# Performance work log

Hardware: AMD Instinct MI355X
Metric: run time of the kernel (lower is better)

The kernel has to match this reference:

```python
import jax, jax.numpy as jnp
import numpy as np
import math

L = 6      # num transformer layers
D = 128    # hidden_dim
H = 8      # heads
C = D // H # per-head dim (concat -> H*C == hidden_dim so residual add works)
F = 9      # node_features
OUT = 3    # output_dim
B, S, NN = 2, 128, 64
N = B * S * NN
E = 262144


def setup_inputs() -> dict:
    key = jax.random.key(0)
    ks = jax.random.split(key, 16)
    sc = 0.02
    g = lambda k, shp: jax.random.normal(k, shp, jnp.float32) * sc

    x = jax.random.normal(ks[0], (N, F), jnp.float32)
    edge_index = jax.random.randint(ks[1], (2, E), 0, N, dtype=jnp.int32)

    # sinusoidal positional encoding buffer [S, D]
    pos = np.arange(S, dtype=np.float32)[:, None]
    div = np.exp(np.arange(0, D, 2, dtype=np.float32) * (-math.log(10000.0) / D))
    pe = np.zeros((S, D), np.float32)
    pe[:, 0::2] = np.sin(pos * div)
    pe[:, 1::2] = np.cos(pos * div)

    return dict(
        x=x, edge_index=edge_index, pe=jnp.asarray(pe),
        Win=g(ks[2], (F, D)), bin_=jnp.zeros((D,), jnp.float32),
        Wq=g(ks[3], (L, D, D)), bq=jnp.zeros((L, D), jnp.float32),
        Wk=g(ks[4], (L, D, D)), bk=jnp.zeros((L, D), jnp.float32),
        Wv=g(ks[5], (L, D, D)), bv=jnp.zeros((L, D), jnp.float32),
        Ws=g(ks[6], (L, D, D)), bs=jnp.zeros((L, D), jnp.float32),
        Wb=g(ks[7], (L, 3 * D, 1)), bb=jnp.zeros((L, 1), jnp.float32),
        ln_g=jnp.ones((L, D), jnp.float32), ln_b=jnp.zeros((L, D), jnp.float32),
        Wo1=g(ks[8], (D, D // 2)), bo1=jnp.zeros((D // 2,), jnp.float32),
        Wo2=g(ks[9], (D // 2, OUT)), bo2=jnp.zeros((OUT,), jnp.float32),
        batch_size=B, seq_len=S, num_nodes=NN,
    )


def _layer_norm(x, g, b, eps=1e-5):
    mu = x.mean(-1, keepdims=True)
    var = ((x - mu) ** 2).mean(-1, keepdims=True)
    return (x - mu) / jnp.sqrt(var + eps) * g + b


def _transformer_conv(h, src, dst, Wq, bq, Wk, bk, Wv, bv, Ws, bs, Wb, bb):
    # PyG TransformerConv (beta=True, concat): edge gather -> per-head dot scores
    # -> scatter-softmax over incoming edges per dst node -> scatter-add aggregate.
    n = h.shape[0]
    q = (h @ Wq + bq).reshape(n, H, C)
    k = (h @ Wk + bk).reshape(n, H, C)
    v = (h @ Wv + bv).reshape(n, H, C)
    scores = jnp.einsum('ehc,ehc->eh', q[dst], k[src]) / math.sqrt(C)  # [E,H]
    m = jax.ops.segment_max(scores, dst, num_segments=n)               # [N,H]
    ex = jnp.exp(scores - jax.lax.stop_gradient(m)[dst])
    denom = jax.ops.segment_sum(ex, dst, num_segments=n)
    alpha = ex / (denom[dst] + 1e-16)                                  # [E,H]
    msg = (v[src] * alpha[:, :, None]).reshape(-1, H * C)              # [E,D]
    agg = jax.ops.segment_sum(msg, dst, num_segments=n)                # [N,D]
    xr = h @ Ws + bs                                                   # skip branch
    beta = jax.nn.sigmoid(jnp.concatenate([agg, xr, agg - xr], -1) @ Wb + bb)
    return beta * xr + (1.0 - beta) * agg


def reference(x, edge_index, pe, Win, bin_, Wq, bq, Wk, bk, Wv, bv, Ws, bs,
              Wb, bb, ln_g, ln_b, Wo1, bo1, Wo2, bo2,
              batch_size, seq_len, num_nodes):
    src, dst = edge_index[0], edge_index[1]
    d = Win.shape[1]
    h = x @ Win + bin_
    # add temporal positional encoding per timestep
    h = (h.reshape(batch_size, seq_len, num_nodes, d)
         + pe[:seq_len][None, :, None, :]).reshape(-1, d)
    for i in range(Wq.shape[0]):
        hn = _transformer_conv(h, src, dst, Wq[i], bq[i], Wk[i], bk[i],
                               Wv[i], bv[i], Ws[i], bs[i], Wb[i], bb[i])
        h = _layer_norm(h + hn, ln_g[i], ln_b[i])
    return jax.nn.relu(h @ Wo1 + bo1) @ Wo2 + bo2
```

## Files before the change

kernel.cpp:

```cpp
#include <hip/hip_runtime.h>

#define NNODES 16384
#define EDGES  262144
#define DH     128
#define NH     8
#define CH     16
#define NL     6
#define SEQ    128
#define NNPG   64

typedef short bf16x8 __attribute__((ext_vector_type(8)));
typedef float f32x4 __attribute__((ext_vector_type(4)));
typedef float f32x2 __attribute__((ext_vector_type(2)));

static __device__ __forceinline__ unsigned short f2bf(float f) {
  unsigned u = __float_as_uint(f);
  u += 0x7FFFu + ((u >> 16) & 1u);
  return (unsigned short)(u >> 16);
}
static __device__ __forceinline__ float bfl(unsigned u) { return __uint_as_float(u << 16); }
static __device__ __forceinline__ float bfh(unsigned u) { return __uint_as_float(u & 0xffff0000u); }

__global__ __launch_bounds__(128) void k_input(const float* __restrict__ x,
    const float* __restrict__ Win, const float* __restrict__ bin,
    const float* __restrict__ pe, float* __restrict__ h,
    unsigned short* __restrict__ hb) {
  const int n = blockIdx.x, d = threadIdx.x;
  __shared__ float xs[9];
  if (d < 9) xs[d] = x[n * 9 + d];
  __syncthreads();
  float acc = bin[d];
#pragma unroll
  for (int f = 0; f < 9; ++f) acc = fmaf(xs[f], Win[f * DH + d], acc);
  const float val = acc + pe[((n / NNPG) % SEQ) * DH + d];
  h[n * DH + d] = val;
  hb[n * DH + d] = f2bf(val);
}

__global__ __launch_bounds__(256) void k_count(const int* __restrict__ ei,
                                               int* __restrict__ cnt) {
  const int e = blockIdx.x * 256 + threadIdx.x;
  atomicAdd(&cnt[ei[EDGES + e]], 1);
}

__global__ __launch_bounds__(1024) void k_scan(int* __restrict__ cnt,
                                               int* __restrict__ row_start) {
  __shared__ int part[1024];
  const int t = threadIdx.x;
  int loc[16];
  int s = 0;
  const int base = t * 16;
#pragma unroll
  for (int i = 0; i < 16; ++i) { loc[i] = cnt[base + i]; s += loc[i]; }
  part[t] = s;
  __syncthreads();
  for (int off = 1; off < 1024; off <<= 1) {
    int add = (t >= off) ? part[t - off] : 0;
    __syncthreads();
    part[t] += add;
    __syncthreads();
  }
  int run = (t == 0) ? 0 : part[t - 1];
#pragma unroll
  for (int i = 0; i < 16; ++i) {
    row_start[base + i] = run;
    run += loc[i];
    cnt[base + i] = 0;
  }
  if (t == 0) row_start[NNODES] = EDGES;
}

__global__ __launch_bounds__(256) void k_fill(const int* __restrict__ ei,
    const int* __restrict__ row_start, int* __restrict__ cursor,
    int* __restrict__ csr_src) {
  const int e = blockIdx.x * 256 + threadIdx.x;
  const int d = ei[EDGES + e];
  csr_src[row_start[d] + atomicAdd(&cursor[d], 1)] = ei[e];
}

__global__ __launch_bounds__(64) void k_wconv(const float* __restrict__ Wq,
    const float* __restrict__ Wk, const float* __restrict__ Wv,
    const float* __restrict__ Ws, unsigned short* __restrict__ Wf) {
  const int bid = blockIdx.x;
  const int layer = bid >> 7, rem = bid & 127;
  const int mat = rem >> 5, tile = rem & 31;
  const int nt = tile >> 2, kt = tile & 3;
  const int lane = threadIdx.x;
  const float* W = ((mat == 0) ? Wq : (mat == 1) ? Wk : (mat == 2) ? Wv : Ws)
                   + layer * DH * DH;
  const int n = nt * 16 + (lane & 15);
  const int k0 = kt * 32 + (lane >> 4) * 8;
  unsigned pk[4];
#pragma unroll
  for (int jj = 0; jj < 4; ++jj) {
    const unsigned lo = f2bf(W[(k0 + 2 * jj) * DH + n]);
    const unsigned hi = f2bf(W[(k0 + 2 * jj + 1) * DH + n]);
    pk[jj] = lo | (hi << 16);
  }
  uint4 o = {pk[0], pk[1], pk[2], pk[3]};
  *(uint4*)&Wf[(((layer * 4 + mat) * 32 + tile) * 64 + lane) * 8] = o;
}

__global__ __launch_bounds__(256) void k_gemm(const unsigned short* __restrict__ hb,
    const unsigned short* __restrict__ Wf,
    const float* __restrict__ bq, const float* __restrict__ bk,
    const float* __restrict__ bv, const float* __restrict__ bs,
    unsigned short* __restrict__ qb, unsigned char* __restrict__ kb8,
    unsigned char* __restrict__ vb8, float* __restrict__ xr) {
  const int mt = blockIdx.x;
  const int wv = threadIdx.x >> 6, lane = threadIdx.x & 63;
  const int g = blockIdx.y * 4 + wv;
  const int mat = g >> 1, nbase = (g & 1) * 64;
  const unsigned short* Wm = Wf + mat * 16384;
  const float* bias = (mat == 0) ? bq : (mat == 1) ? bk : (mat == 2) ? bv : bs;
  const int m0 = lane & 15, quad = lane >> 4;
  const int nt0 = (g & 1) * 4;

  const f32x4 z = {0.f, 0.f, 0.f, 0.f};
  f32x4 acc[2][4] = {{z, z, z, z}, {z, z, z, z}};
#pragma unroll
  for (int kt = 0; kt < 4; ++kt) {
    const bf16x8 a0 = *(const bf16x8*)&hb[(mt * 32 + m0) * DH + kt * 32 + quad * 8];
    const bf16x8 a1 = *(const bf16x8*)&hb[(mt * 32 + 16 + m0) * DH + kt * 32 + quad * 8];
#pragma unroll
    for (int j = 0; j < 4; ++j) {
      const bf16x8 b = *(const bf16x8*)&Wm[(((nt0 + j) * 4 + kt) * 64 + lane) * 8];
      acc[0][j] = __builtin_amdgcn_mfma_f32_16x16x32_bf16(a0, b, acc[0][j], 0, 0, 0);
      acc[1][j] = __builtin_amdgcn_mfma_f32_16x16x32_bf16(a1, b, acc[1][j], 0, 0, 0);
    }
  }
  unsigned char* __restrict__ f8dst = (mat == 1) ? kb8 : vb8;
#pragma unroll
  for (int half = 0; half < 2; ++half) {
#pragma unroll
    for (int j = 0; j < 4; ++j) {
      const int col = nbase + j * 16 + m0;
      const float bvv = bias[col];
#pragma unroll
      for (int r = 0; r < 4; ++r) {
        const float val = acc[half][j][r] + bvv;
        const int row = mt * 32 + half * 16 + quad * 4 + r;
        if (mat == 0) {
          qb[row * DH + col] = f2bf(val);
        } else if (mat == 3) {
          xr[row * DH + col] = val;
        } else {
          const float nbv = __shfl_xor(val, 1);
          if ((lane & 1) == 0) {
            const int pk = __builtin_amdgcn_cvt_pk_fp8_f32(val, nbv, 0, false);
            *(unsigned short*)&f8dst[row * DH + col] = (unsigned short)pk;
          }
        }
      }
    }
  }
}

__device__ __forceinline__ void load16bf(const unsigned short* __restrict__ p, float* r) {
  const uint4 a = *(const uint4*)p;
  const uint4 b = *(const uint4*)(p + 8);
  r[0] = bfl(a.x); r[1] = bfh(a.x); r[2] = bfl(a.y); r[3] = bfh(a.y);
  r[4] = bfl(a.z); r[5] = bfh(a.z); r[6] = bfl(a.w); r[7] = bfh(a.w);
  r[8] = bfl(b.x); r[9] = bfh(b.x); r[10] = bfl(b.y); r[11] = bfh(b.y);
  r[12] = bfl(b.z); r[13] = bfh(b.z); r[14] = bfl(b.w); r[15] = bfh(b.w);
}

__device__ __forceinline__ void decode16f8(const uint4 u, float* r) {
  f32x2 t;
  t = __builtin_amdgcn_cvt_pk_f32_fp8(u.x, false); r[0] = t[0]; r[1] = t[1];
  t = __builtin_amdgcn_cvt_pk_f32_fp8(u.x, true);  r[2] = t[0]; r[3] = t[1];
  t = __builtin_amdgcn_cvt_pk_f32_fp8(u.y, false); r[4] = t[0]; r[5] = t[1];
  t = __builtin_amdgcn_cvt_pk_f32_fp8(u.y, true);  r[6] = t[0]; r[7] = t[1];
  t = __builtin_amdgcn_cvt_pk_f32_fp8(u.z, false); r[8] = t[0]; r[9] = t[1];
  t = __builtin_amdgcn_cvt_pk_f32_fp8(u.z, true);  r[10] = t[0]; r[11] = t[1];
  t = __builtin_amdgcn_cvt_pk_f32_fp8(u.w, false); r[12] = t[0]; r[13] = t[1];
  t = __builtin_amdgcn_cvt_pk_f32_fp8(u.w, true);  r[14] = t[0]; r[15] = t[1];
}

__device__ __forceinline__ void edge_acc_m(const uint4 ku, const uint4 vu, bool valid,
    const float* __restrict__ qr, float* __restrict__ acc, float& denom) {
  float kr[16], vr[16];
  decode16f8(ku, kr);
  float dot = 0.f;
#pragma unroll
  for (int c = 0; c < 16; ++c) dot = fmaf(qr[c], kr[c], dot);
  const float ex = valid ? __expf(dot * 0.25f) : 0.f;
  denom += ex;
  decode16f8(vu, vr);
#pragma unroll
  for (int c = 0; c < 16; ++c) acc[c] = fmaf(ex, vr[c], acc[c]);
}

__global__ __launch_bounds__(256) void k_attn_epi(const unsigned short* __restrict__ qb,
    const unsigned char* __restrict__ kb8, const unsigned char* __restrict__ vb8,
    const int* __restrict__ row_start, const int* __restrict__ csr_src,
    float* __restrict__ h, unsigned short* __restrict__ hb,
    const float* __restrict__ xr,
    const float* __restrict__ Wb, const float* __restrict__ bb,
    const float* __restrict__ ln_g, const float* __restrict__ ln_b) {
  const int wv = threadIdx.x >> 6, lane = threadIdx.x & 63;
  const int n = blockIdx.x * 4 + wv;
  const int es = lane >> 3, hd = lane & 7;
  const int beg = row_start[n], end = row_start[n + 1];
  int j = beg + es;
  int idx[4];
#pragma unroll
  for (int t = 0; t < 4; ++t) {
    const int jt = j + 8 * t;
    idx[t] = (jt < end) ? csr_src[jt] : -1;
  }
  float qr[16];
  load16bf(&qb[n * DH + hd * CH], qr);
  uint4 kf[4], vf[4];
#pragma unroll
  for (int t = 0; t < 4; ++t) {
    const int s = (idx[t] >= 0) ? idx[t] : 0;
    kf[t] = *(const uint4*)&kb8[s * DH + hd * CH];
    vf[t] = *(const uint4*)&vb8[s * DH + hd * CH];
  }
  float acc[16] = {};
  float denom = 0.f;
#pragma unroll
  for (int t = 0; t < 4; ++t)
    edge_acc_m(kf[t], vf[t], idx[t] >= 0, qr, acc, denom);
  for (j = beg + es + 32; j < end; j += 8) {
    const int s = csr_src[j];
    const uint4 ku = *(const uint4*)&kb8[s * DH + hd * CH];
    const uint4 vu = *(const uint4*)&vb8[s * DH + hd * CH];
    edge_acc_m(ku, vu, true, qr, acc, denom);
  }
#pragma unroll
  for (int off = 8; off <= 32; off <<= 1) {
    denom += __shfl_xor(denom, off);
#pragma unroll
    for (int c = 0; c < 16; ++c) acc[c] += __shfl_xor(acc[c], off);
  }
  const float inv = 1.f / (denom + 1e-16f);
  float o0 = 0.f, o1 = 0.f;
#pragma unroll
  for (int c = 0; c < 8; ++c) {
    if (es == c) { o0 = acc[2 * c]; o1 = acc[2 * c + 1]; }
  }
  const int d0 = hd * CH + es * 2;
  const float ax = o0 * inv, ay = o1 * inv;
  const float2 r = *(const float2*)&xr[n * DH + d0];
  const float2 w0 = *(const float2*)&Wb[d0];
  const float2 w1 = *(const float2*)&Wb[DH + d0];
  const float2 w2 = *(const float2*)&Wb[2 * DH + d0];
  float p = ax * w0.x + ay * w0.y + r.x * w1.x + r.y * w1.y
          + (ax - r.x) * w2.x + (ay - r.y) * w2.y;
#pragma unroll
  for (int off = 1; off <= 32; off <<= 1) p += __shfl_xor(p, off);
  const float beta = 1.f / (1.f + __expf(-(p + bb[0])));
  const float2 hv = *(const float2*)&h[n * DH + d0];
  const float t0 = hv.x + beta * r.x + (1.f - beta) * ax;
  const float t1 = hv.y + beta * r.y + (1.f - beta) * ay;
  float sum = t0 + t1, sq = t0 * t0 + t1 * t1;
#pragma unroll
  for (int off = 1; off <= 32; off <<= 1) {
    sum += __shfl_xor(sum, off);
    sq  += __shfl_xor(sq, off);
  }
  const float mu = sum * (1.f / DH);
  const float rinv = rsqrtf(sq * (1.f / DH) - mu * mu + 1e-5f);
  const float2 g = *(const float2*)&ln_g[d0];
  const float2 b = *(const float2*)&ln_b[d0];
  float2 o = {(t0 - mu) * rinv * g.x + b.x, (t1 - mu) * rinv * g.y + b.y};
  *(float2*)&h[n * DH + d0] = o;
  const unsigned lo = f2bf(o.x), hi = f2bf(o.y);
  *(unsigned*)&hb[n * DH + d0] = lo | (hi << 16);
}

__global__ __launch_bounds__(256) void k_final(const float* __restrict__ h,
    const float* __restrict__ Wo1, const float* __restrict__ bo1,
    const float* __restrict__ Wo2, const float* __restrict__ bo2,
    float* __restrict__ out) {
  __shared__ float hs[4][DH];
  const int lane = threadIdx.x & 63, wid = threadIdx.x >> 6;
  const int n = blockIdx.x * 4 + wid;
  const float2 hv = *(const float2*)&h[n * DH + lane * 2];
  hs[wid][lane * 2] = hv.x;
  hs[wid][lane * 2 + 1] = hv.y;
  __syncthreads();
  float m = bo1[lane];
#pragma unroll 16
  for (int d = 0; d < DH; ++d) m = fmaf(hs[wid][d], Wo1[d * 64 + lane], m);
  m = fmaxf(m, 0.f);
  float o0 = m * Wo2[lane * 3 + 0];
  float o1 = m * Wo2[lane * 3 + 1];
  float o2 = m * Wo2[lane * 3 + 2];
#pragma unroll
  for (int off = 32; off; off >>= 1) {
    o0 += __shfl_xor(o0, off);
    o1 += __shfl_xor(o1, off);
    o2 += __shfl_xor(o2, off);
  }
  if (lane == 0) {
    out[n * 3 + 0] = o0 + bo2[0];
    out[n * 3 + 1] = o1 + bo2[1];
    out[n * 3 + 2] = o2 + bo2[2];
  }
}

extern "C" void kernel_launch(void* const* d_in, const int* in_sizes, int n_in,
                              void* d_out, int out_size, void* d_ws, size_t ws_size,
                              hipStream_t stream) {
  const float* x   = (const float*)d_in[0];
  const int*   ei  = (const int*)d_in[1];
  const float* pe  = (const float*)d_in[2];
  const float* Win = (const float*)d_in[3];
  const float* bin = (const float*)d_in[4];
  const float* Wq  = (const float*)d_in[5];
  const float* bq  = (const float*)d_in[6];
  const float* Wk  = (const float*)d_in[7];
  const float* bk  = (const float*)d_in[8];
  const float* Wv  = (const float*)d_in[9];
  const float* bv  = (const float*)d_in[10];
  const float* Wsk = (const float*)d_in[11];
  const float* bs  = (const float*)d_in[12];
  const float* Wb  = (const float*)d_in[13];
  const float* bb  = (const float*)d_in[14];
  const float* lng = (const float*)d_in[15];
  const float* lnb = (const float*)d_in[16];
  const float* Wo1 = (const float*)d_in[17];
  const float* bo1 = (const float*)d_in[18];
  const float* Wo2 = (const float*)d_in[19];
  const float* bo2 = (const float*)d_in[20];

  const size_t NU = (size_t)NNODES * DH;
  char* base = (char*)d_ws;
  float* h   = (float*)base;                  base += NU * 4;
  float* xr  = (float*)base;                  base += NU * 4;
  unsigned short* hb = (unsigned short*)base; base += NU * 2;
  unsigned short* qb = (unsigned short*)base; base += NU * 2;
  unsigned char* kb8 = (unsigned char*)base;  base += NU;
  unsigned char* vb8 = (unsigned char*)base;  base += NU;
  unsigned short* Wf = (unsigned short*)base; base += (size_t)NL * 4 * 16384 * 2;
  int* row_start = (int*)base;                base += (NNODES + 1) * 4;
  int* cnt       = (int*)base;                base += NNODES * 4;
  int* csr_src   = (int*)base;

  (void)hipMemsetAsync(cnt, 0, NNODES * sizeof(int), stream);
  k_count<<<EDGES / 256, 256, 0, stream>>>(ei, cnt);
  k_scan<<<1, 1024, 0, stream>>>(cnt, row_start);
  k_fill<<<EDGES / 256, 256, 0, stream>>>(ei, row_start, cnt, csr_src);
  k_wconv<<<NL * 128, 64, 0, stream>>>(Wq, Wk, Wv, Wsk, Wf);
  k_input<<<NNODES, 128, 0, stream>>>(x, Win, bin, pe, h, hb);
  for (int l = 0; l < NL; ++l) {
    k_gemm<<<dim3(NNODES / 32, 2), 256, 0, stream>>>(
        hb, Wf + (size_t)l * 4 * 16384,
        bq + l * DH, bk + l * DH, bv + l * DH, bs + l * DH, qb, kb8, vb8, xr);
    k_attn_epi<<<NNODES / 4, 256, 0, stream>>>(qb, kb8, vb8, row_start, csr_src,
                                               h, hb, xr, Wb + l * 3 * DH, bb + l,
                                               lng + l * DH, lnb + l * DH);
  }
  k_final<<<NNODES / 4, 256, 0, stream>>>(h, Wo1, bo1, Wo2, bo2, (float*)d_out);
}
```

Measured before the change: 390.5 us.

## Split edge score computation into a separate edge-parallel kernel

Edge attention scores (q·k and exp) move out of the per-destination-node attention kernel into a new k_score kernel that runs in parallel over CSR edges, using a new csr_dst array built in k_fill. Scores go to a global buffer of E×H floats, which the aggregation kernel reads back while gathering V. The aim is to balance load across edges rather than nodes with uneven degree. The cost is an extra launch per layer and an 8 MB round-trip of scores through memory.

```diff
diff --git a/kernel.cpp b/kernel.cpp
--- a/kernel.cpp
+++ b/kernel.cpp
@@ -72,10 +72,12 @@
 
 __global__ __launch_bounds__(256) void k_fill(const int* __restrict__ ei,
     const int* __restrict__ row_start, int* __restrict__ cursor,
-    int* __restrict__ csr_src) {
+    int* __restrict__ csr_src, int* __restrict__ csr_dst) {
   const int e = blockIdx.x * 256 + threadIdx.x;
   const int d = ei[EDGES + e];
-  csr_src[row_start[d] + atomicAdd(&cursor[d], 1)] = ei[e];
+  const int pos = row_start[d] + atomicAdd(&cursor[d], 1);
+  csr_src[pos] = ei[e];
+  csr_dst[pos] = d;
 }
 
 __global__ __launch_bounds__(64) void k_wconv(const float* __restrict__ Wq,
@@ -177,22 +179,35 @@
   t = __builtin_amdgcn_cvt_pk_f32_fp8(u.w, true);  r[14] = t[0]; r[15] = t[1];
 }
 
-__device__ __forceinline__ void edge_acc_m(const uint4 ku, const uint4 vu, bool valid,
-    const float* __restrict__ qr, float* __restrict__ acc, float& denom) {
-  float kr[16], vr[16];
+__global__ __launch_bounds__(256) void k_score(const unsigned short* __restrict__ qb,
+    const unsigned char* __restrict__ kb8, const int* __restrict__ csr_src,
+    const int* __restrict__ csr_dst, float* __restrict__ ex) {
+  const int wv = threadIdx.x >> 6, lane = threadIdx.x & 63;
+  const int el = lane >> 3, hd = lane & 7;
+  const int j = blockIdx.x * 32 + wv * 8 + el;
+  const int s = csr_src[j];
+  const int d = csr_dst[j];
+  float qr[16], kr[16];
+  load16bf(&qb[d * DH + hd * CH], qr);
+  const uint4 ku = *(const uint4*)&kb8[s * DH + hd * CH];
   decode16f8(ku, kr);
   float dot = 0.f;
 #pragma unroll
   for (int c = 0; c < 16; ++c) dot = fmaf(qr[c], kr[c], dot);
-  const float ex = valid ? __expf(dot * 0.25f) : 0.f;
-  denom += ex;
+  ex[j * 8 + hd] = __expf(dot * 0.25f);
+}
+
+__device__ __forceinline__ void v_acc(const uint4 vu, float w,
+    float* __restrict__ acc, float& denom) {
+  float vr[16];
   decode16f8(vu, vr);
-#pragma unroll
-  for (int c = 0; c < 16; ++c) acc[c] = fmaf(ex, vr[c], acc[c]);
-}
-
-__global__ __launch_bounds__(256) void k_attn_epi(const unsigned short* __restrict__ qb,
-    const unsigned char* __restrict__ kb8, const unsigned char* __restrict__ vb8,
+  denom += w;
+#pragma unroll
+  for (int c = 0; c < 16; ++c) acc[c] = fmaf(w, vr[c], acc[c]);
+}
+
+__global__ __launch_bounds__(256) void k_attn_epi(
+    const unsigned char* __restrict__ vb8, const float* __restrict__ ex,
     const int* __restrict__ row_start, const int* __restrict__ csr_src,
     float* __restrict__ h, unsigned short* __restrict__ hb,
     const float* __restrict__ xr,
@@ -202,32 +217,30 @@
   const int n = blockIdx.x * 4 + wv;
   const int es = lane >> 3, hd = lane & 7;
   const int beg = row_start[n], end = row_start[n + 1];
-  int j = beg + es;
+  const int j0 = beg + es;
   int idx[4];
 #pragma unroll
   for (int t = 0; t < 4; ++t) {
-    const int jt = j + 8 * t;
+    const int jt = j0 + 8 * t;
     idx[t] = (jt < end) ? csr_src[jt] : -1;
   }
-  float qr[16];
-  load16bf(&qb[n * DH + hd * CH], qr);
-  uint4 kf[4], vf[4];
+  float w[4];
+  uint4 vf[4];
 #pragma unroll
   for (int t = 0; t < 4; ++t) {
+    const int jt = j0 + 8 * t;
+    w[t] = (idx[t] >= 0) ? ex[jt * 8 + hd] : 0.f;
     const int s = (idx[t] >= 0) ? idx[t] : 0;
-    kf[t] = *(const uint4*)&kb8[s * DH + hd * CH];
     vf[t] = *(const uint4*)&vb8[s * DH + hd * CH];
   }
   float acc[16] = {};
   float denom = 0.f;
 #pragma unroll
-  for (int t = 0; t < 4; ++t)
-    edge_acc_m(kf[t], vf[t], idx[t] >= 0, qr, acc, denom);
-  for (j = beg + es + 32; j < end; j += 8) {
+  for (int t = 0; t < 4; ++t) v_acc(vf[t], w[t], acc, denom);
+  for (int j = j0 + 32; j < end; j += 8) {
     const int s = csr_src[j];
-    const uint4 ku = *(const uint4*)&kb8[s * DH + hd * CH];
     const uint4 vu = *(const uint4*)&vb8[s * DH + hd * CH];
-    edge_acc_m(ku, vu, true, qr, acc, denom);
+    v_acc(vu, ex[j * 8 + hd], acc, denom);
   }
 #pragma unroll
   for (int off = 8; off <= 32; off <<= 1) {
@@ -336,21 +349,24 @@
   unsigned char* kb8 = (unsigned char*)base;  base += NU;
   unsigned char* vb8 = (unsigned char*)base;  base += NU;
   unsigned short* Wf = (unsigned short*)base; base += (size_t)NL * 4 * 16384 * 2;
+  float* ex = (float*)base;                   base += (size_t)EDGES * NH * 4;
   int* row_start = (int*)base;                base += (NNODES + 1) * 4;
   int* cnt       = (int*)base;                base += NNODES * 4;
-  int* csr_src   = (int*)base;
+  int* csr_src   = (int*)base;                base += EDGES * 4;
+  int* csr_dst   = (int*)base;
 
   (void)hipMemsetAsync(cnt, 0, NNODES * sizeof(int), stream);
   k_count<<<EDGES / 256, 256, 0, stream>>>(ei, cnt);
   k_scan<<<1, 1024, 0, stream>>>(cnt, row_start);
-  k_fill<<<EDGES / 256, 256, 0, stream>>>(ei, row_start, cnt, csr_src);
+  k_fill<<<EDGES / 256, 256, 0, stream>>>(ei, row_start, cnt, csr_src, csr_dst);
   k_wconv<<<NL * 128, 64, 0, stream>>>(Wq, Wk, Wv, Wsk, Wf);
   k_input<<<NNODES, 128, 0, stream>>>(x, Win, bin, pe, h, hb);
   for (int l = 0; l < NL; ++l) {
     k_gemm<<<dim3(NNODES / 32, 2), 256, 0, stream>>>(
         hb, Wf + (size_t)l * 4 * 16384,
         bq + l * DH, bk + l * DH, bv + l * DH, bs + l * DH, qb, kb8, vb8, xr);
-    k_attn_epi<<<NNODES / 4, 256, 0, stream>>>(qb, kb8, vb8, row_start, csr_src,
+    k_score<<<EDGES / 32, 256, 0, stream>>>(qb, kb8, csr_src, csr_dst, ex);
+    k_attn_epi<<<NNODES / 4, 256, 0, stream>>>(vb8, ex, row_start, csr_src,
                                                h, hb, xr, Wb + l * 3 * DH, bb + l,
                                                lng + l * DH, lnb + l * DH);
   }
```

Result: slower. 417.9 us (+7.0%).
